# Performance work log

Hardware: AMD Instinct MI355X
Metric: run time of the kernel (lower is better)

Reference implementation:

```python
import jax, jax.numpy as jnp
import numpy as np

B, S, R, C_MSA, C_PAIR, H, D = 1, 128, 384, 256, 128, 8, 32
EPS = 1e-5


def setup_inputs() -> dict:
    key = jax.random.key(0)
    ks = jax.random.split(key, 8)
    w = 0.02
    return {
        "msa_repr": jax.random.normal(ks[0], (B, S, R, C_MSA), jnp.float32),
        "pair_repr": jax.random.normal(ks[1], (B, R, R, C_PAIR), jnp.float32),
        "ln_g": jnp.ones((R,), jnp.float32),
        "ln_b": jnp.zeros((R,), jnp.float32),
        "Wq": jax.random.normal(ks[2], (C_MSA, H * D), jnp.float32) * w,
        "Wk": jax.random.normal(ks[3], (C_MSA, H * D), jnp.float32) * w,
        "Wv": jax.random.normal(ks[4], (C_MSA, H * D), jnp.float32) * w,
        "Wb": jax.random.normal(ks[5], (C_PAIR, H), jnp.float32) * w,
        "bb": jnp.zeros((H,), jnp.float32),
        "Wg": jax.random.normal(ks[6], (C_MSA, H * D), jnp.float32) * w,
        "bg": jnp.zeros((H * D,), jnp.float32),
        "Wo": jax.random.normal(ks[7], (H * D, C_MSA), jnp.float32) * w,
        "bo": jnp.zeros((C_MSA,), jnp.float32),
    }


def reference(msa_repr, pair_repr, ln_g, ln_b, Wq, Wk, Wv, Wb, bb, Wg, bg, Wo, bo):
    b, s, r, c = msa_repr.shape
    scale = 1.0 / jnp.sqrt(jnp.float32(D))
    # LayerNorm over the residue axis r (module permutes b s r c -> b c s r and
    # normalizes the last dim = sequence_size), gamma/beta indexed by r.
    mu = jnp.mean(msa_repr, axis=2, keepdims=True)
    var = jnp.var(msa_repr, axis=2, keepdims=True)
    x = (msa_repr - mu) * jax.lax.rsqrt(var + EPS)
    x = x * ln_g[None, None, :, None] + ln_b[None, None, :, None]
    # flatten MSA rows into batch: (b*s, r, c)
    x = x.reshape(b * s, r, c)
    q = (x @ Wq).reshape(b * s, r, H, D).transpose(0, 2, 1, 3)  # (bs) h r d
    k = (x @ Wk).reshape(b * s, r, H, D).transpose(0, 2, 1, 3)
    v = (x @ Wv).reshape(b * s, r, H, D).transpose(0, 2, 1, 3)
    g = jax.nn.sigmoid(x @ Wg + bg).reshape(b * s, r, H, D).transpose(0, 2, 1, 3)
    # pair bias: b i j c -> b i j h -> b h i j, tiled over rows as in einops repeat '(a b)'
    bias = (pair_repr @ Wb + bb).transpose(0, 3, 1, 2)  # b h i j
    bias = jnp.tile(bias, (s, 1, 1, 1))  # (s*b) h i j (matches original (a b) order)
    dots = jnp.einsum('bhid,bhjd->bhij', q, k)  # (bs) h r r  -- dominant memory traffic
    attn = jax.nn.softmax(scale * dots + bias, axis=-1)
    out = jnp.einsum('bhij,bhjd->bhid', attn, v) * g  # (bs) h r d
    # '(b h) n w d -> b h w n d' with h=s, then concat heads along last dim
    out = out.reshape(b, s, H, r, D).transpose(0, 1, 3, 2, 4).reshape(b, s, r, H * D)
    return out @ Wo + bo  # b s r c
```

## Files before the change

kernel.cpp:

```cpp
#include <hip/hip_runtime.h>
#include <hip/hip_bf16.h>
#include <stdint.h>

typedef __attribute__((ext_vector_type(8))) short s16x8;
typedef __attribute__((ext_vector_type(4))) float f32x4;
typedef __attribute__((ext_vector_type(2))) float f32x2;

#define AS1(p) ((const __attribute__((address_space(1))) void*)(p))
#define AS3(p) ((__attribute__((address_space(3))) void*)(p))

__device__ __forceinline__ ushort f2bf(float f){
  union { float f; uint32_t u; } v; v.f = f;
  uint32_t r = v.u + 0x7FFFu + ((v.u >> 16) & 1u);
  return (ushort)(r >> 16);
}
__device__ __forceinline__ float bf2f(ushort u){
  union { uint32_t u; float f; } v; v.u = ((uint32_t)u) << 16; return v.f;
}

__global__ __launch_bounds__(256) void ln_part(const float* __restrict__ msa,
    float* __restrict__ part){
  int s = blockIdx.x, rq = blockIdx.y, c = threadIdx.x;
  const float* p = msa + (size_t)s*98304 + (size_t)rq*48*256 + c;
  float sum = 0.f, sq = 0.f;
  for (int r = 0; r < 48; ++r){ float v = p[(size_t)r*256]; sum += v; sq += v*v; }
  f32x2* o = (f32x2*)part;
  o[((size_t)s*8 + rq)*256 + c] = (f32x2){sum, sq};
}

__global__ __launch_bounds__(256) void ln_stats(const float* __restrict__ part,
    float* __restrict__ stats){
  int s = blockIdx.x, c = threadIdx.x;
  const f32x2* p = (const f32x2*)part;
  float sum = 0.f, sq = 0.f;
  #pragma unroll
  for (int rq = 0; rq < 8; ++rq){
    f32x2 v = p[((size_t)s*8 + rq)*256 + c];
    sum += v.x; sq += v.y;
  }
  float mu = sum * (1.f/384.f);
  float var = sq * (1.f/384.f) - mu*mu;
  ((f32x2*)stats)[(size_t)s*256 + c] = (f32x2){mu, rsqrtf(var + 1e-5f)};
}

__global__ __launch_bounds__(256) void ln_apply(const float* __restrict__ msa,
    const float* __restrict__ stats, const float* __restrict__ ln_g,
    const float* __restrict__ ln_b, ushort* __restrict__ xbf){
  int s = blockIdx.x, rq = blockIdx.y, c = threadIdx.x;
  f32x2 st = ((const f32x2*)stats)[(size_t)s*256 + c];
  const float* p = msa + (size_t)s*98304 + (size_t)rq*48*256 + c;
  ushort* o = xbf + (size_t)s*98304 + (size_t)rq*48*256 + c;
  for (int r = 0; r < 48; ++r){
    int rr = rq*48 + r;
    float v = (p[(size_t)r*256] - st.x) * st.y * ln_g[rr] + ln_b[rr];
    o[(size_t)r*256] = f2bf(v);
  }
}

__global__ __launch_bounds__(256) void cvt_w(const float* __restrict__ Wq, const float* __restrict__ Wk,
    const float* __restrict__ Wv, const float* __restrict__ Wg, const float* __restrict__ Wo,
    ushort* __restrict__ out){
  int w = blockIdx.y;
  const float* W = (w==0)?Wq:(w==1)?Wk:(w==2)?Wv:(w==3)?Wg:Wo;
  int idx = blockIdx.x*256 + threadIdx.x;
  int k = idx >> 8, n = idx & 255;
  out[(size_t)w*65536 + (size_t)n*256 + k] = f2bf(W[idx]);
}

__global__ __launch_bounds__(256) void bias_kernel(const float* __restrict__ pair,
    const float* __restrict__ Wb, const float* __restrict__ bb, float* __restrict__ bias){
  __shared__ float pl[32*133];
  __shared__ float wb[128*8];
  int i = blockIdx.x, j0 = blockIdx.y*32, tid = threadIdx.x;
  for (int t = tid; t < 1024; t += 256) wb[t] = Wb[t];
  const float* src = pair + ((size_t)i*384 + j0)*128;
  for (int t = tid; t < 4096; t += 256){ int j = t>>7, c = t&127; pl[j*133 + c] = src[t]; }
  __syncthreads();
  int h = tid >> 5, jj = tid & 31;
  float acc = bb[h];
  const float* row = pl + jj*133;
  #pragma unroll 8
  for (int c = 0; c < 128; ++c) acc = fmaf(row[c], wb[c*8 + h], acc);
  bias[(size_t)h*147456 + (size_t)i*384 + (j0 + jj)] = acc;
}

__device__ __forceinline__ void stage_a64(const ushort* __restrict__ A, int m0,
                                          ushort* Al, int tid){
  int wave = tid>>6, lane = tid&63;
  #pragma unroll
  for (int it = 0; it < 8; ++it){
    int chunk = wave*8 + it;
    int base  = chunk*1024;
    int beta  = base + lane*16;
    int row   = beta>>9, cbs = beta&511;
    int cb    = cbs ^ ((row&7)<<4);
    const char* src = (const char*)A + (size_t)(m0+row)*512 + cb;
    __builtin_amdgcn_global_load_lds(AS1(src), AS3((char*)Al + base), 16, 0, 0);
  }
}

__device__ __forceinline__ void gemm64_lds(const ushort* Al, const ushort* __restrict__ Bt,
                                           int lr, int lg, f32x4 acc[4][4]){
  #pragma unroll
  for (int ks = 0; ks < 8; ++ks){
    s16x8 a[4], b[4];
    #pragma unroll
    for (int mt = 0; mt < 4; ++mt){
      int row = mt*16 + lr;
      int beta = row*512 + ((ks*64 + lg*16) ^ ((lr&7)<<4));
      a[mt] = *reinterpret_cast<const s16x8*>((const char*)Al + beta);
    }
    #pragma unroll
    for (int nt = 0; nt < 4; ++nt)
      b[nt] = *reinterpret_cast<const s16x8*>(Bt + (size_t)(nt*16 + lr)*256 + ks*32 + lg*8);
    #pragma unroll
    for (int mt = 0; mt < 4; ++mt)
      #pragma unroll
      for (int nt = 0; nt < 4; ++nt)
        acc[mt][nt] = __builtin_amdgcn_mfma_f32_16x16x32_bf16(a[mt], b[nt], acc[mt][nt], 0, 0, 0);
  }
}

__global__ __launch_bounds__(256, 4) void proj_kernel(const ushort* __restrict__ xbf,
    const ushort* __restrict__ wt_all, const float* __restrict__ bg,
    ushort* __restrict__ q, ushort* __restrict__ k, ushort* __restrict__ v, ushort* __restrict__ g){
  __shared__ ushort Al[64*256];
  int w = blockIdx.y;
  const ushort* Bt = wt_all + (size_t)w*65536;
  int tid = threadIdx.x, wave = tid>>6, lane = tid&63, lr = lane&15, lg = lane>>4;
  int m0 = blockIdx.x*64;
  stage_a64(xbf, m0, Al, tid);
  __syncthreads();
  f32x4 acc[4][4];
  #pragma unroll
  for (int a=0;a<4;++a) for (int b=0;b<4;++b) acc[a][b] = (f32x4){0.f,0.f,0.f,0.f};
  gemm64_lds(Al, Bt + (size_t)(wave*64)*256, lr, lg, acc);
  ushort* out = (w==0)?q:(w==1)?k:(w==2)?v:g;
  #pragma unroll
  for (int mt = 0; mt < 4; ++mt){
    int mrow = m0 + mt*16 + lg*4;
    int s = mrow/384, r = mrow - s*384;
    #pragma unroll
    for (int nt = 0; nt < 4; ++nt){
      int n = wave*64 + nt*16 + lr;
      int hh = n>>5, d = n&31;
      size_t o = (((size_t)s*8 + hh)*384 + r)*32 + d;
      #pragma unroll
      for (int t = 0; t < 4; ++t){
        float val = acc[mt][nt][t];
        if (w == 3) val = 1.0f/(1.0f + __expf(-(val + bg[n])));
        out[o + (size_t)t*32] = f2bf(val);
      }
    }
  }
}

#define VSTR 400
__global__ __launch_bounds__(512) void attn_kernel(const ushort* __restrict__ q,
    const ushort* __restrict__ kk, const ushort* __restrict__ vv, const ushort* __restrict__ gg,
    const float* __restrict__ bias, ushort* __restrict__ att_out){
  __shared__ ushort Kl[384*40];
  __shared__ ushort Vt[32*VSTR];
  const float SCALE = 0.17677669529663687f;
  int s = blockIdx.x, h = blockIdx.y, tid = threadIdx.x;
  const size_t base = ((size_t)s*8 + h)*384*32;
  for (int it = 0; it < 3; ++it){
    int idx = tid + it*512;
    int r = idx>>2, d0 = (idx&3)*8;
    int m = r>>5, a = (r>>3)&3, j = r&7;
    int rho = (2*m + (j>>2))*16 + 4*a + (j&3);
    s16x8 val = *reinterpret_cast<const s16x8*>(kk + base + (size_t)r*32 + d0);
    *reinterpret_cast<s16x8*>(&Kl[rho*40 + d0]) = val;
  }
  for (int it = 0; it < 3; ++it){
    int idx = tid + it*512;
    int r = idx>>2, d0 = (idx&3)*8;
    s16x8 val = *reinterpret_cast<const s16x8*>(vv + base + (size_t)r*32 + d0);
    #pragma unroll
    for (int j = 0; j < 8; ++j) Vt[(d0+j)*VSTR + r] = ((ushort*)&val)[j];
  }
  __syncthreads();
  int wave = tid>>6, lane = tid&63, lr = lane&15, lg = lane>>4;
  for (int itile = wave; itile < 24; itile += 8){
    int i0 = itile*16;
    s16x8 qf = *reinterpret_cast<const s16x8*>(q + base + (size_t)(i0 + lr)*32 + lg*8);
    const float* bp = bias + (size_t)h*147456 + (size_t)(i0 + lr)*384 + 8*lg;
    f32x4 acc0 = {0.f,0.f,0.f,0.f}, acc1 = {0.f,0.f,0.f,0.f};
    float rsum = 0.f;
    #pragma unroll 4
    for (int m = 0; m < 12; ++m){
      s16x8 kf0 = *reinterpret_cast<const s16x8*>(&Kl[((2*m+0)*16 + lr)*40 + lg*8]);
      s16x8 kf1 = *reinterpret_cast<const s16x8*>(&Kl[((2*m+1)*16 + lr)*40 + lg*8]);
      f32x4 d0 = __builtin_amdgcn_mfma_f32_16x16x32_bf16(kf0, qf, (f32x4){0.f,0.f,0.f,0.f}, 0, 0, 0);
      f32x4 d1 = __builtin_amdgcn_mfma_f32_16x16x32_bf16(kf1, qf, (f32x4){0.f,0.f,0.f,0.f}, 0, 0, 0);
      f32x4 bv0 = *reinterpret_cast<const f32x4*>(bp + 32*m);
      f32x4 bv1 = *reinterpret_cast<const f32x4*>(bp + 32*m + 4);
      s16x8 pa;
      #pragma unroll
      for (int t = 0; t < 4; ++t){
        float e0 = __expf(fmaf(d0[t], SCALE, bv0[t]));
        float e1 = __expf(fmaf(d1[t], SCALE, bv1[t]));
        rsum += e0 + e1;
        ((ushort*)&pa)[t]   = f2bf(e0);
        ((ushort*)&pa)[t+4] = f2bf(e1);
      }
      s16x8 vb0 = *reinterpret_cast<const s16x8*>(&Vt[lr*VSTR + 32*m + 8*lg]);
      s16x8 vb1 = *reinterpret_cast<const s16x8*>(&Vt[(16+lr)*VSTR + 32*m + 8*lg]);
      acc0 = __builtin_amdgcn_mfma_f32_16x16x32_bf16(pa, vb0, acc0, 0, 0, 0);
      acc1 = __builtin_amdgcn_mfma_f32_16x16x32_bf16(pa, vb1, acc1, 0, 0, 0);
    }
    rsum += __shfl_xor(rsum, 16);
    rsum += __shfl_xor(rsum, 32);
    const ushort* gp = gg + base + (size_t)(i0 + lg*4)*32;
    ushort* op = att_out + ((size_t)s*384 + i0 + lg*4)*256 + h*32;
    #pragma unroll
    for (int t = 0; t < 4; ++t){
      float inv = 1.0f / __shfl(rsum, 4*lg + t);
      float g0 = bf2f(gp[(size_t)t*32 + lr]);
      float g1 = bf2f(gp[(size_t)t*32 + 16 + lr]);
      op[(size_t)t*256 + lr]      = f2bf(acc0[t]*inv*g0);
      op[(size_t)t*256 + 16 + lr] = f2bf(acc1[t]*inv*g1);
    }
  }
}

__global__ __launch_bounds__(256, 4) void oproj_kernel(const ushort* __restrict__ att,
    const ushort* __restrict__ Wot, const float* __restrict__ bo, float* __restrict__ out){
  __shared__ ushort Al[64*256];
  int tid = threadIdx.x, wave = tid>>6, lane = tid&63, lr = lane&15, lg = lane>>4;
  int m0 = blockIdx.x*64;
  stage_a64(att, m0, Al, tid);
  __syncthreads();
  f32x4 acc[4][4];
  #pragma unroll
  for (int a=0;a<4;++a) for (int b=0;b<4;++b) acc[a][b] = (f32x4){0.f,0.f,0.f,0.f};
  gemm64_lds(Al, Wot + (size_t)(wave*64)*256, lr, lg, acc);
  #pragma unroll
  for (int mt = 0; mt < 4; ++mt){
    int mrow = m0 + mt*16 + lg*4;
    #pragma unroll
    for (int nt = 0; nt < 4; ++nt){
      int n = wave*64 + nt*16 + lr;
      float bn = bo[n];
      #pragma unroll
      for (int t = 0; t < 4; ++t)
        out[(size_t)(mrow + t)*256 + n] = acc[mt][nt][t] + bn;
    }
  }
}

extern "C" void kernel_launch(void* const* d_in, const int* in_sizes, int n_in,
                              void* d_out, int out_size, void* d_ws, size_t ws_size,
                              hipStream_t stream){
  const float* msa  = (const float*)d_in[0];
  const float* pair = (const float*)d_in[1];
  const float* ln_g = (const float*)d_in[2];
  const float* ln_b = (const float*)d_in[3];
  const float* Wq   = (const float*)d_in[4];
  const float* Wk   = (const float*)d_in[5];
  const float* Wv   = (const float*)d_in[6];
  const float* Wb   = (const float*)d_in[7];
  const float* bb   = (const float*)d_in[8];
  const float* Wg   = (const float*)d_in[9];
  const float* bg   = (const float*)d_in[10];
  const float* Wo   = (const float*)d_in[11];
  const float* bo   = (const float*)d_in[12];
  float* out = (float*)d_out;
  char* ws = (char*)d_ws;
  const size_t SZ = (size_t)49152*256*2;
  ushort* xbf = (ushort*)(ws);
  ushort* qb  = (ushort*)(ws + SZ);
  ushort* kb  = (ushort*)(ws + 2*SZ);
  ushort* vb  = (ushort*)(ws + 3*SZ);
  ushort* gb  = (ushort*)(ws + 4*SZ);
  float*  bias= (float*)(ws + 5*SZ);
  ushort* wt  = (ushort*)(ws + 5*SZ + 4718592);
  ushort* att = xbf;
  float* part  = (float*)(ws + SZ);
  float* stats = (float*)(ws + SZ + 4*1024*1024);

  ln_part  <<<dim3(128,8),  dim3(256), 0, stream>>>(msa, part);
  ln_stats <<<dim3(128),    dim3(256), 0, stream>>>(part, stats);
  ln_apply <<<dim3(128,8),  dim3(256), 0, stream>>>(msa, stats, ln_g, ln_b, xbf);
  cvt_w      <<<dim3(256,5),   dim3(256), 0, stream>>>(Wq, Wk, Wv, Wg, Wo, wt);
  bias_kernel<<<dim3(384,12),  dim3(256), 0, stream>>>(pair, Wb, bb, bias);
  proj_kernel<<<dim3(768,4),   dim3(256), 0, stream>>>(xbf, wt, bg, qb, kb, vb, gb);
  attn_kernel<<<dim3(128,8),   dim3(512), 0, stream>>>(qb, kb, vb, gb, bias, att);
  oproj_kernel<<<dim3(768),    dim3(256), 0, stream>>>(att, wt + (size_t)4*65536, bo, out);
}
```

Before: 389.3 us.

## Pre-permute K and pre-transpose V in projection, use exp2 and packed bf16 converts

The projection kernel now writes K already in the row order the attention MFMA expects and writes V transposed (d-major), so the attention kernel reads K fragments straight from global memory and stages V into LDS with vector copies instead of scalar transposing stores. The log2(e) factor is folded into the pair bias and the score scale, so the softmax uses raw v_exp_f32 and v_cvt_pk_bf16_f32 packing. The aim is to cut LDS staging cost and ALU work in the softmax inner loop, and raise occupancy (launch bounds 512,8; smaller LDS). The cost is uncoalesced scattered K stores and 8-byte strided V stores in the projection, and K reloads from global/L2 for every query tile.

```diff
diff --git a/kernel.cpp b/kernel.cpp
--- a/kernel.cpp
+++ b/kernel.cpp
@@ -16,6 +16,20 @@
 }
 __device__ __forceinline__ float bf2f(ushort u){
   union { uint32_t u; float f; } v; v.u = ((uint32_t)u) << 16; return v.f;
+}
+__device__ __forceinline__ float exp2_fast(float x){
+  float r;
+  asm("v_exp_f32 %0, %1\n\ts_nop 0" : "=v"(r) : "v"(x));
+  return r;
+}
+__device__ __forceinline__ uint32_t cvt_pk_bf16(float lo, float hi){
+  uint32_t r;
+  asm("v_cvt_pk_bf16_f32 %0, %1, %2" : "=v"(r) : "v"(lo), "v"(hi));
+  return r;
+}
+__device__ __forceinline__ int rho_of(int r){
+  int m = r>>5, a = (r>>3)&3, j = r&7;
+  return (2*m + (j>>2))*16 + 4*a + (j&3);
 }
 
 __global__ __launch_bounds__(256) void ln_part(const float* __restrict__ msa,
@@ -81,7 +95,7 @@
   const float* row = pl + jj*133;
   #pragma unroll 8
   for (int c = 0; c < 128; ++c) acc = fmaf(row[c], wb[c*8 + h], acc);
-  bias[(size_t)h*147456 + (size_t)i*384 + (j0 + jj)] = acc;
+  bias[(size_t)h*147456 + (size_t)i*384 + (j0 + jj)] = acc * 1.4426950408889634f;
 }
 
 __device__ __forceinline__ void stage_a64(const ushort* __restrict__ A, int m0,
@@ -135,49 +149,51 @@
   #pragma unroll
   for (int a=0;a<4;++a) for (int b=0;b<4;++b) acc[a][b] = (f32x4){0.f,0.f,0.f,0.f};
   gemm64_lds(Al, Bt + (size_t)(wave*64)*256, lr, lg, acc);
-  ushort* out = (w==0)?q:(w==1)?k:(w==2)?v:g;
   #pragma unroll
   for (int mt = 0; mt < 4; ++mt){
     int mrow = m0 + mt*16 + lg*4;
-    int s = mrow/384, r = mrow - s*384;
+    int s = mrow/384, rbase = mrow - s*384;
     #pragma unroll
     for (int nt = 0; nt < 4; ++nt){
       int n = wave*64 + nt*16 + lr;
       int hh = n>>5, d = n&31;
-      size_t o = (((size_t)s*8 + hh)*384 + r)*32 + d;
-      #pragma unroll
-      for (int t = 0; t < 4; ++t){
-        float val = acc[mt][nt][t];
-        if (w == 3) val = 1.0f/(1.0f + __expf(-(val + bg[n])));
-        out[o + (size_t)t*32] = f2bf(val);
+      if (w == 2){
+        uint32_t lo = cvt_pk_bf16(acc[mt][nt][0], acc[mt][nt][1]);
+        uint32_t hi = cvt_pk_bf16(acc[mt][nt][2], acc[mt][nt][3]);
+        *reinterpret_cast<uint2*>(&v[(((size_t)s*8 + hh)*32 + d)*384 + rbase]) = make_uint2(lo, hi);
+      } else if (w == 1){
+        #pragma unroll
+        for (int t = 0; t < 4; ++t)
+          k[(((size_t)s*8 + hh)*384 + rho_of(rbase + t))*32 + d] = f2bf(acc[mt][nt][t]);
+      } else {
+        ushort* out = (w==0) ? q : g;
+        size_t o = (((size_t)s*8 + hh)*384 + rbase)*32 + d;
+        #pragma unroll
+        for (int t = 0; t < 4; ++t){
+          float val = acc[mt][nt][t];
+          if (w == 3) val = 1.0f/(1.0f + __expf(-(val + bg[n])));
+          out[o + (size_t)t*32] = f2bf(val);
+        }
       }
     }
   }
 }
 
-#define VSTR 400
-__global__ __launch_bounds__(512) void attn_kernel(const ushort* __restrict__ q,
-    const ushort* __restrict__ kk, const ushort* __restrict__ vv, const ushort* __restrict__ gg,
+#define VSTR 392
+__global__ __launch_bounds__(512, 8) void attn_kernel(const ushort* __restrict__ q,
+    const ushort* __restrict__ kk, const ushort* __restrict__ vt, const ushort* __restrict__ gg,
     const float* __restrict__ bias, ushort* __restrict__ att_out){
-  __shared__ ushort Kl[384*40];
   __shared__ ushort Vt[32*VSTR];
-  const float SCALE = 0.17677669529663687f;
+  const float SC2 = 0.17677669529663687f * 1.4426950408889634f;
   int s = blockIdx.x, h = blockIdx.y, tid = threadIdx.x;
   const size_t base = ((size_t)s*8 + h)*384*32;
+  const ushort* vsrc = vt + base;
+  #pragma unroll
   for (int it = 0; it < 3; ++it){
-    int idx = tid + it*512;
-    int r = idx>>2, d0 = (idx&3)*8;
-    int m = r>>5, a = (r>>3)&3, j = r&7;
-    int rho = (2*m + (j>>2))*16 + 4*a + (j&3);
-    s16x8 val = *reinterpret_cast<const s16x8*>(kk + base + (size_t)r*32 + d0);
-    *reinterpret_cast<s16x8*>(&Kl[rho*40 + d0]) = val;
-  }
-  for (int it = 0; it < 3; ++it){
-    int idx = tid + it*512;
-    int r = idx>>2, d0 = (idx&3)*8;
-    s16x8 val = *reinterpret_cast<const s16x8*>(vv + base + (size_t)r*32 + d0);
-    #pragma unroll
-    for (int j = 0; j < 8; ++j) Vt[(d0+j)*VSTR + r] = ((ushort*)&val)[j];
+    int c = tid + it*512;
+    int d = c/48, rem = c - d*48;
+    s16x8 val = *reinterpret_cast<const s16x8*>(vsrc + (size_t)d*384 + rem*8);
+    *reinterpret_cast<s16x8*>(&Vt[d*VSTR + rem*8]) = val;
   }
   __syncthreads();
   int wave = tid>>6, lane = tid&63, lr = lane&15, lg = lane>>4;
@@ -185,30 +201,38 @@
     int i0 = itile*16;
     s16x8 qf = *reinterpret_cast<const s16x8*>(q + base + (size_t)(i0 + lr)*32 + lg*8);
     const float* bp = bias + (size_t)h*147456 + (size_t)(i0 + lr)*384 + 8*lg;
+    const ushort* kp = kk + base + (size_t)lr*32 + lg*8;
     f32x4 acc0 = {0.f,0.f,0.f,0.f}, acc1 = {0.f,0.f,0.f,0.f};
-    float rsum = 0.f;
+    float rsA = 0.f, rsB = 0.f;
     #pragma unroll 4
     for (int m = 0; m < 12; ++m){
-      s16x8 kf0 = *reinterpret_cast<const s16x8*>(&Kl[((2*m+0)*16 + lr)*40 + lg*8]);
-      s16x8 kf1 = *reinterpret_cast<const s16x8*>(&Kl[((2*m+1)*16 + lr)*40 + lg*8]);
+      s16x8 kf0 = *reinterpret_cast<const s16x8*>(kp + (size_t)(2*m+0)*512);
+      s16x8 kf1 = *reinterpret_cast<const s16x8*>(kp + (size_t)(2*m+1)*512);
       f32x4 d0 = __builtin_amdgcn_mfma_f32_16x16x32_bf16(kf0, qf, (f32x4){0.f,0.f,0.f,0.f}, 0, 0, 0);
       f32x4 d1 = __builtin_amdgcn_mfma_f32_16x16x32_bf16(kf1, qf, (f32x4){0.f,0.f,0.f,0.f}, 0, 0, 0);
       f32x4 bv0 = *reinterpret_cast<const f32x4*>(bp + 32*m);
       f32x4 bv1 = *reinterpret_cast<const f32x4*>(bp + 32*m + 4);
-      s16x8 pa;
-      #pragma unroll
-      for (int t = 0; t < 4; ++t){
-        float e0 = __expf(fmaf(d0[t], SCALE, bv0[t]));
-        float e1 = __expf(fmaf(d1[t], SCALE, bv1[t]));
-        rsum += e0 + e1;
-        ((ushort*)&pa)[t]   = f2bf(e0);
-        ((ushort*)&pa)[t+4] = f2bf(e1);
-      }
+      float e00 = exp2_fast(fmaf(d0[0], SC2, bv0[0]));
+      float e01 = exp2_fast(fmaf(d0[1], SC2, bv0[1]));
+      float e02 = exp2_fast(fmaf(d0[2], SC2, bv0[2]));
+      float e03 = exp2_fast(fmaf(d0[3], SC2, bv0[3]));
+      float e10 = exp2_fast(fmaf(d1[0], SC2, bv1[0]));
+      float e11 = exp2_fast(fmaf(d1[1], SC2, bv1[1]));
+      float e12 = exp2_fast(fmaf(d1[2], SC2, bv1[2]));
+      float e13 = exp2_fast(fmaf(d1[3], SC2, bv1[3]));
+      rsA += (e00 + e01) + (e02 + e03);
+      rsB += (e10 + e11) + (e12 + e13);
+      union { uint32_t u[4]; s16x8 v; } pa;
+      pa.u[0] = cvt_pk_bf16(e00, e01);
+      pa.u[1] = cvt_pk_bf16(e02, e03);
+      pa.u[2] = cvt_pk_bf16(e10, e11);
+      pa.u[3] = cvt_pk_bf16(e12, e13);
       s16x8 vb0 = *reinterpret_cast<const s16x8*>(&Vt[lr*VSTR + 32*m + 8*lg]);
       s16x8 vb1 = *reinterpret_cast<const s16x8*>(&Vt[(16+lr)*VSTR + 32*m + 8*lg]);
-      acc0 = __builtin_amdgcn_mfma_f32_16x16x32_bf16(pa, vb0, acc0, 0, 0, 0);
-      acc1 = __builtin_amdgcn_mfma_f32_16x16x32_bf16(pa, vb1, acc1, 0, 0, 0);
-    }
+      acc0 = __builtin_amdgcn_mfma_f32_16x16x32_bf16(pa.v, vb0, acc0, 0, 0, 0);
+      acc1 = __builtin_amdgcn_mfma_f32_16x16x32_bf16(pa.v, vb1, acc1, 0, 0, 0);
+    }
+    float rsum = rsA + rsB;
     rsum += __shfl_xor(rsum, 16);
     rsum += __shfl_xor(rsum, 32);
     const ushort* gp = gg + base + (size_t)(i0 + lg*4)*32;
```

Result: slower. 419.5 us (+7.8%).
